# Kernel tuning notes

Hardware: AMD Instinct MI355X
Metric: run time of the kernel (lower is better)

## Reference

```python
import jax, jax.numpy as jnp
import numpy as np

SENSOR_H, SENSOR_W = 256, 256
SPP = 16
BATCH, C, H_IMG, W_IMG = 4, 3, 1024, 1024


def setup_inputs() -> dict:
    key = jax.random.key(0)
    k1, k2 = jax.random.split(key)
    img = jax.random.uniform(k1, (BATCH, C, H_IMG, W_IMG), dtype=jnp.float32)
    jitter = jax.random.uniform(k2, (SPP, SENSOR_H, SENSOR_W, 2), dtype=jnp.float32)
    t = jnp.ones((1,), jnp.float32)
    return {"img": img, "t": t, "jitter": jitter}


def deform(pos, t):
    # Analytic per-axis foveation diffeomorphism [-1,1]^2 -> [-1,1]^2:
    #   f(u) = tanh(t*u)/tanh(t), f'(u) = t*(1 - tanh(t*u)^2)/tanh(t)
    # Jacobian is diagonal, so det = f'(x) * f'(y).
    tt = t[0]
    s = jnp.tanh(tt)
    th = jnp.tanh(tt * pos)
    warped = th / s                      # (..., 2)
    dd = tt * (1.0 - th * th) / s        # diagonal Jacobian entries (..., 2)
    det = dd[..., 0] * dd[..., 1]        # (...)
    return warped, det


def grid_sample_border(img, grid):
    # img: (b,c,H,W); grid: (spp,h,w,2) in [-1,1]
    # bilinear, padding_mode='border', align_corners=False (matches F.grid_sample)
    b, c, H, W = img.shape
    gx = (grid[..., 0] + 1.0) * (W / 2.0) - 0.5
    gy = (grid[..., 1] + 1.0) * (H / 2.0) - 0.5
    gx = jnp.clip(gx, 0.0, W - 1.0)
    gy = jnp.clip(gy, 0.0, H - 1.0)
    x0 = jnp.floor(gx)
    y0 = jnp.floor(gy)
    wx = (gx - x0)[None, None]           # (1,1,spp,h,w)
    wy = (gy - y0)[None, None]
    x0i = jnp.clip(x0.astype(jnp.int32), 0, W - 1)
    y0i = jnp.clip(y0.astype(jnp.int32), 0, H - 1)
    x1i = jnp.clip(x0i + 1, 0, W - 1)
    y1i = jnp.clip(y0i + 1, 0, H - 1)
    # fancy-index gather: result (b,c,spp,h,w); avoids tiling img over (b*spp)
    v00 = img[:, :, y0i, x0i]
    v01 = img[:, :, y0i, x1i]
    v10 = img[:, :, y1i, x0i]
    v11 = img[:, :, y1i, x1i]
    return (v00 * (1 - wx) * (1 - wy) + v01 * wx * (1 - wy)
            + v10 * (1 - wx) * wy + v11 * wx * wy)


def reference(img, t, jitter):
    step_x = 2.0 / SENSOR_W
    step_y = 2.0 / SENSOR_H
    px = jnp.arange(-1.0, 1.0, step_x, dtype=jnp.float32)
    py = jnp.arange(-1.0, 1.0, step_y, dtype=jnp.float32)
    gx, gy = jnp.meshgrid(px, py, indexing='xy')          # (h, w)
    pixel_pos = jnp.stack((gx, gy), axis=-1)[None]        # (1, h, w, 2)
    jit = jitter * jnp.array([step_x, step_y], jnp.float32)
    pos = pixel_pos + jit                                 # (spp, h, w, 2)
    warped, det = deform(pos, t)                          # (spp,h,w,2), (spp,h,w)
    samples = grid_sample_border(img, warped)             # (b, c, spp, h, w)
    weighted = jnp.mean(samples * det[None, None], axis=2)  # (b, c, h, w)
    area = jnp.mean(det, axis=0)[None, None]              # (1, 1, h, w)
    return weighted / area
```

## Files before the change

### kernel.cpp

```cpp
#include <hip/hip_runtime.h>
#include <hip/hip_fp16.h>

#define SPP   16
#define SH    256
#define SW    256
#define HI    1024
#define WI    1024
#define CH    3
#define BATCH 4

#define TS    8
#define MAXD  46
#define PLN   2176
#define NITER 34
#define NTHR  64

#define AS1C(p) ((const __attribute__((address_space(1))) void*)(p))
#define AS3(p)  ((__attribute__((address_space(3))) void*)(p))

__device__ __forceinline__ float fast_tanh(float x) {
    const float e = __expf(2.0f * x);
    return (e - 1.0f) * __builtin_amdgcn_rcpf(e + 1.0f);
}

__global__ __launch_bounds__(NTHR, 4) void foveated_wave8(
    const float* __restrict__ img,
    const float* __restrict__ t_ptr,
    const float* __restrict__ jitter,
    float* __restrict__ out)
{
    __shared__ float lds_f[CH][PLN];

    const int bid  = blockIdx.x;
    const int L    = (bid & 7) * 512 + (bid >> 3);
    const int b    = L >> 10;
    const int rem  = L & 1023;
    const int trow = rem >> 5;
    const int tcol = rem & 31;
    const int sx0  = tcol * TS;
    const int sy0  = trow * TS;

    const int lane = threadIdx.x;
    const int sx   = sx0 + (lane & 7);
    const int sy   = sy0 + (lane >> 3);

    const float step  = 2.0f / 256.0f;
    const float tt    = t_ptr[0];
    const float inv_s = __builtin_amdgcn_rcpf(fast_tanh(tt));

    auto gmap = [&](float p) {
        float g = (fast_tanh(tt * p) * inv_s + 1.0f) * 512.0f - 0.5f;
        return fminf(fmaxf(g, 0.0f), 1023.0f);
    };
    const float pxmin = -1.0f + sx0 * step, pxmax = pxmin + TS * step;
    const float pymin = -1.0f + sy0 * step, pymax = pymin + TS * step;
    const int x_lo = max((int)gmap(pxmin) - 1, 0);
    const int x_hi = min((int)gmap(pxmax) + 2, WI - 1);
    const int y_lo = max((int)gmap(pymin) - 1, 0);
    const int y_hi = min((int)gmap(pymax) + 2, HI - 1);
    const int ncols = x_hi - x_lo + 1;
    const int nrows = y_hi - y_lo + 1;
    const bool fits = (ncols > 0) && (nrows > 0) &&
                      (ncols <= MAXD) && (nrows <= MAXD);

    const size_t plane = (size_t)HI * WI;
    const float* __restrict__ p0 = img + (size_t)(b * CH) * plane;
    const float* __restrict__ p1 = p0 + plane;
    const float* __restrict__ p2 = p1 + plane;

    const float px = -1.0f + sx * step;
    const float py = -1.0f + sy * step;

    const float2* __restrict__ jit2 = (const float2*)jitter;
    const int jbase = sy * SW + sx;
    const float2 jv0  = jit2[jbase +  0 * (SH * SW)];
    const float2 jv1  = jit2[jbase +  1 * (SH * SW)];
    const float2 jv2  = jit2[jbase +  2 * (SH * SW)];
    const float2 jv3  = jit2[jbase +  3 * (SH * SW)];
    const float2 jv4  = jit2[jbase +  4 * (SH * SW)];
    const float2 jv5  = jit2[jbase +  5 * (SH * SW)];
    const float2 jv6  = jit2[jbase +  6 * (SH * SW)];
    const float2 jv7  = jit2[jbase +  7 * (SH * SW)];
    const float2 jv8  = jit2[jbase +  8 * (SH * SW)];
    const float2 jv9  = jit2[jbase +  9 * (SH * SW)];
    const float2 jv10 = jit2[jbase + 10 * (SH * SW)];
    const float2 jv11 = jit2[jbase + 11 * (SH * SW)];
    const float2 jv12 = jit2[jbase + 12 * (SH * SW)];
    const float2 jv13 = jit2[jbase + 13 * (SH * SW)];
    const float2 jv14 = jit2[jbase + 14 * (SH * SW)];
    const float2 jv15 = jit2[jbase + 15 * (SH * SW)];

    float acc0 = 0.0f, acc1 = 0.0f, acc2 = 0.0f, dsum = 0.0f;

    float* __restrict__ P0 = &lds_f[0][0];
    float* __restrict__ P1 = &lds_f[1][0];
    float* __restrict__ P2 = &lds_f[2][0];

    auto sample_lds = [&](float jx, float jy) {
        const float posx = px + jx * step;
        const float posy = py + jy * step;

        const float thx = fast_tanh(tt * posx);
        const float thy = fast_tanh(tt * posy);
        const float ddx = tt * (1.0f - thx * thx) * inv_s;
        const float ddy = tt * (1.0f - thy * thy) * inv_s;
        const float det = ddx * ddy;

        float gx = (thx * inv_s + 1.0f) * 512.0f - 0.5f;
        float gy = (thy * inv_s + 1.0f) * 512.0f - 0.5f;
        gx = fminf(fmaxf(gx, 0.0f), (float)(WI - 1));
        gy = fminf(fmaxf(gy, 0.0f), (float)(HI - 1));

        const int xb = min((int)gx, WI - 2);
        const int yb = min((int)gy, HI - 2);
        const float fx = gx - (float)xb;
        const float fy = gy - (float)yb;

        const float w00 = (1.0f - fx) * (1.0f - fy) * det;
        const float w01 = fx * (1.0f - fy) * det;
        const float w10 = (1.0f - fx) * fy * det;
        const float w11 = fx * fy * det;
        dsum += det;

        const int lidx = (yb - y_lo) * ncols + (xb - x_lo);
        const int l10  = lidx + ncols;

        acc0 += w00 * P0[lidx] + w01 * P0[lidx + 1] + w10 * P0[l10] + w11 * P0[l10 + 1];
        acc1 += w00 * P1[lidx] + w01 * P1[lidx + 1] + w10 * P1[l10] + w11 * P1[l10 + 1];
        acc2 += w00 * P2[lidx] + w01 * P2[lidx + 1] + w10 * P2[l10] + w11 * P2[l10 + 1];
    };

    auto sample_glb = [&](float jx, float jy) {
        const float posx = px + jx * step;
        const float posy = py + jy * step;

        const float thx = fast_tanh(tt * posx);
        const float thy = fast_tanh(tt * posy);
        const float ddx = tt * (1.0f - thx * thx) * inv_s;
        const float ddy = tt * (1.0f - thy * thy) * inv_s;
        const float det = ddx * ddy;

        float gx = (thx * inv_s + 1.0f) * 512.0f - 0.5f;
        float gy = (thy * inv_s + 1.0f) * 512.0f - 0.5f;
        gx = fminf(fmaxf(gx, 0.0f), (float)(WI - 1));
        gy = fminf(fmaxf(gy, 0.0f), (float)(HI - 1));

        const int xb = min((int)gx, WI - 2);
        const int yb = min((int)gy, HI - 2);
        const float fx = gx - (float)xb;
        const float fy = gy - (float)yb;

        const float w00 = (1.0f - fx) * (1.0f - fy) * det;
        const float w01 = fx * (1.0f - fy) * det;
        const float w10 = (1.0f - fx) * fy * det;
        const float w11 = fx * fy * det;
        dsum += det;

        const int i0 = yb * WI + xb;
        const int i1 = i0 + WI;
        { const float a0 = p0[i0], a1 = p0[i0 + 1], c0 = p0[i1], c1 = p0[i1 + 1];
          acc0 += a0 * w00 + a1 * w01 + c0 * w10 + c1 * w11; }
        { const float a0 = p1[i0], a1 = p1[i0 + 1], c0 = p1[i1], c1 = p1[i1 + 1];
          acc1 += a0 * w00 + a1 * w01 + c0 * w10 + c1 * w11; }
        { const float a0 = p2[i0], a1 = p2[i0 + 1], c0 = p2[i1], c1 = p2[i1 + 1];
          acc2 += a0 * w00 + a1 * w01 + c0 * w10 + c1 * w11; }
    };

    if (fits) {
        const int npix  = nrows * ncols;
        const int niter = (npix + 63) >> 6;
        const unsigned mdiv = (1u << 22) / (unsigned)ncols + 1u;
        #pragma unroll
        for (int k = 0; k < NITER; ++k) {
            if (k < niter) {
                int i = k * 64 + lane;
                i = min(i, npix - 1);
                const int r = (int)(((unsigned)i * mdiv) >> 22);
                const int c = i - r * ncols;
                const int g = (y_lo + r) * WI + (x_lo + c);
                __builtin_amdgcn_global_load_lds(AS1C(p0 + g), AS3(P0 + k * 64), 4, 0, 0);
                __builtin_amdgcn_global_load_lds(AS1C(p1 + g), AS3(P1 + k * 64), 4, 0, 0);
                __builtin_amdgcn_global_load_lds(AS1C(p2 + g), AS3(P2 + k * 64), 4, 0, 0);
            }
        }
        asm volatile("s_waitcnt vmcnt(0)" ::: "memory");
        __builtin_amdgcn_sched_barrier(0);

        sample_lds(jv0.x,  jv0.y);   sample_lds(jv1.x,  jv1.y);
        sample_lds(jv2.x,  jv2.y);   sample_lds(jv3.x,  jv3.y);
        sample_lds(jv4.x,  jv4.y);   sample_lds(jv5.x,  jv5.y);
        sample_lds(jv6.x,  jv6.y);   sample_lds(jv7.x,  jv7.y);
        sample_lds(jv8.x,  jv8.y);   sample_lds(jv9.x,  jv9.y);
        sample_lds(jv10.x, jv10.y);  sample_lds(jv11.x, jv11.y);
        sample_lds(jv12.x, jv12.y);  sample_lds(jv13.x, jv13.y);
        sample_lds(jv14.x, jv14.y);  sample_lds(jv15.x, jv15.y);
    } else {
        sample_glb(jv0.x,  jv0.y);   sample_glb(jv1.x,  jv1.y);
        sample_glb(jv2.x,  jv2.y);   sample_glb(jv3.x,  jv3.y);
        sample_glb(jv4.x,  jv4.y);   sample_glb(jv5.x,  jv5.y);
        sample_glb(jv6.x,  jv6.y);   sample_glb(jv7.x,  jv7.y);
        sample_glb(jv8.x,  jv8.y);   sample_glb(jv9.x,  jv9.y);
        sample_glb(jv10.x, jv10.y);  sample_glb(jv11.x, jv11.y);
        sample_glb(jv12.x, jv12.y);  sample_glb(jv13.x, jv13.y);
        sample_glb(jv14.x, jv14.y);  sample_glb(jv15.x, jv15.y);
    }

    const float inv_d = 1.0f / dsum;
    const int pix = sy * SW + sx;
    const size_t ob = (size_t)b * CH * (SH * SW) + pix;
    out[ob]                 = acc0 * inv_d;
    out[ob + (SH * SW)]     = acc1 * inv_d;
    out[ob + 2 * (SH * SW)] = acc2 * inv_d;
}

extern "C" void kernel_launch(void* const* d_in, const int* in_sizes, int n_in,
                              void* d_out, int out_size, void* d_ws, size_t ws_size,
                              hipStream_t stream) {
    const float* img    = (const float*)d_in[0];
    const float* t      = (const float*)d_in[1];
    const float* jitter = (const float*)d_in[2];
    float* out          = (float*)d_out;

    hipLaunchKernelGGL(foveated_wave8, dim3(4096), dim3(NTHR), 0, stream,
                       img, t, jitter, out);
}
```

Before: 103.5 us.

## Stage image tile in LDS as fp16 via register double-buffered loads

Swaps the direct global-to-LDS async copies for ordinary global loads into registers. These are converted to fp16 and stored as a packed half2 R/G plane plus a half B plane, which halves the LDS footprint per block. Loads are software-pipelined in two register batches of eight so conversion overlaps outstanding fetches. Launch bounds drop from 4 to 3 waves per EU. The aim is more resident blocks and fewer LDS bytes per sample, at the cost of fp16 rounding of image values, extra VGPR pressure and conversion ALU work.

```diff
diff --git a/kernel.cpp b/kernel.cpp
--- a/kernel.cpp
+++ b/kernel.cpp
@@ -11,25 +11,22 @@
 
 #define TS    8
 #define MAXD  46
-#define PLN   2176
-#define NITER 34
+#define NPAD  2176
 #define NTHR  64
-
-#define AS1C(p) ((const __attribute__((address_space(1))) void*)(p))
-#define AS3(p)  ((__attribute__((address_space(3))) void*)(p))
 
 __device__ __forceinline__ float fast_tanh(float x) {
     const float e = __expf(2.0f * x);
     return (e - 1.0f) * __builtin_amdgcn_rcpf(e + 1.0f);
 }
 
-__global__ __launch_bounds__(NTHR, 4) void foveated_wave8(
+__global__ __launch_bounds__(NTHR, 3) void foveated_hocc8(
     const float* __restrict__ img,
     const float* __restrict__ t_ptr,
     const float* __restrict__ jitter,
     float* __restrict__ out)
 {
-    __shared__ float lds_f[CH][PLN];
+    __shared__ __half2 RG[NPAD];
+    __shared__ __half  B [NPAD];
 
     const int bid  = blockIdx.x;
     const int L    = (bid & 7) * 512 + (bid >> 3);
@@ -92,10 +89,6 @@
 
     float acc0 = 0.0f, acc1 = 0.0f, acc2 = 0.0f, dsum = 0.0f;
 
-    float* __restrict__ P0 = &lds_f[0][0];
-    float* __restrict__ P1 = &lds_f[1][0];
-    float* __restrict__ P2 = &lds_f[2][0];
-
     auto sample_lds = [&](float jx, float jy) {
         const float posx = px + jx * step;
         const float posy = py + jy * step;
@@ -125,9 +118,18 @@
         const int lidx = (yb - y_lo) * ncols + (xb - x_lo);
         const int l10  = lidx + ncols;
 
-        acc0 += w00 * P0[lidx] + w01 * P0[lidx + 1] + w10 * P0[l10] + w11 * P0[l10 + 1];
-        acc1 += w00 * P1[lidx] + w01 * P1[lidx + 1] + w10 * P1[l10] + w11 * P1[l10 + 1];
-        acc2 += w00 * P2[lidx] + w01 * P2[lidx + 1] + w10 * P2[l10] + w11 * P2[l10 + 1];
+        const float2 f00 = __half22float2(RG[lidx]);
+        const float2 f01 = __half22float2(RG[lidx + 1]);
+        const float2 f10 = __half22float2(RG[l10]);
+        const float2 f11 = __half22float2(RG[l10 + 1]);
+        const float v00 = __half2float(B[lidx]);
+        const float v01 = __half2float(B[lidx + 1]);
+        const float v10 = __half2float(B[l10]);
+        const float v11 = __half2float(B[l10 + 1]);
+
+        acc0 += w00 * f00.x + w01 * f01.x + w10 * f10.x + w11 * f11.x;
+        acc1 += w00 * f00.y + w01 * f01.y + w10 * f10.y + w11 * f11.y;
+        acc2 += w00 * v00   + w01 * v01   + w10 * v10   + w11 * v11;
     };
 
     auto sample_glb = [&](float jx, float jy) {
@@ -170,20 +172,50 @@
         const int npix  = nrows * ncols;
         const int niter = (npix + 63) >> 6;
         const unsigned mdiv = (1u << 22) / (unsigned)ncols + 1u;
-        #pragma unroll
-        for (int k = 0; k < NITER; ++k) {
-            if (k < niter) {
-                int i = k * 64 + lane;
-                i = min(i, npix - 1);
-                const int r = (int)(((unsigned)i * mdiv) >> 22);
-                const int c = i - r * ncols;
-                const int g = (y_lo + r) * WI + (x_lo + c);
-                __builtin_amdgcn_global_load_lds(AS1C(p0 + g), AS3(P0 + k * 64), 4, 0, 0);
-                __builtin_amdgcn_global_load_lds(AS1C(p1 + g), AS3(P1 + k * 64), 4, 0, 0);
-                __builtin_amdgcn_global_load_lds(AS1C(p2 + g), AS3(P2 + k * 64), 4, 0, 0);
+
+        float arA[8], agA[8], abA[8];
+        float arB[8], agB[8], abB[8];
+
+        #define ISSUE(K, CNT, VR, VG, VB)                                   \
+            if ((K) * 8 < niter) {                                          \
+                _Pragma("unroll")                                           \
+                for (int u = 0; u < (CNT); ++u) {                           \
+                    const int it = (K) * 8 + u;                             \
+                    const int ic = min(it * 64 + lane, npix - 1);           \
+                    const int rr = (int)(((unsigned)ic * mdiv) >> 22);      \
+                    const int cc = ic - rr * ncols;                         \
+                    const int g  = (y_lo + rr) * WI + (x_lo + cc);          \
+                    VR[u] = p0[g];                                          \
+                    VG[u] = p1[g];                                          \
+                    VB[u] = p2[g];                                          \
+                }                                                           \
             }
-        }
-        asm volatile("s_waitcnt vmcnt(0)" ::: "memory");
+
+        #define COMMIT(K, CNT, VR, VG, VB)                                  \
+            if ((K) * 8 < niter) {                                          \
+                _Pragma("unroll")                                           \
+                for (int u = 0; u < (CNT); ++u) {                           \
+                    const int i = ((K) * 8 + u) * 64 + lane;                \
+                    RG[i] = __floats2half2_rn(VR[u], VG[u]);                \
+                    B [i] = __float2half_rn(VB[u]);                         \
+                }                                                           \
+            }
+
+        ISSUE (0, 8, arA, agA, abA);
+        ISSUE (1, 8, arB, agB, abB);
+        COMMIT(0, 8, arA, agA, abA);
+        ISSUE (2, 8, arA, agA, abA);
+        COMMIT(1, 8, arB, agB, abB);
+        ISSUE (3, 8, arB, agB, abB);
+        COMMIT(2, 8, arA, agA, abA);
+        ISSUE (4, 2, arA, agA, abA);
+        COMMIT(3, 8, arB, agB, abB);
+        COMMIT(4, 2, arA, agA, abA);
+
+        #undef ISSUE
+        #undef COMMIT
+
+        asm volatile("s_waitcnt lgkmcnt(0)" ::: "memory");
         __builtin_amdgcn_sched_barrier(0);
 
         sample_lds(jv0.x,  jv0.y);   sample_lds(jv1.x,  jv1.y);
@@ -221,6 +253,6 @@
     const float* jitter = (const float*)d_in[2];
     float* out          = (float*)d_out;
 
-    hipLaunchKernelGGL(foveated_wave8, dim3(4096), dim3(NTHR), 0, stream,
+    hipLaunchKernelGGL(foveated_hocc8, dim3(4096), dim3(NTHR), 0, stream,
                        img, t, jitter, out);
 }
```

Result: slower. 106.5 us (+2.9%).

## Stage full image rows per sensor row in fp16 LDS with vector loads

Applied to the files above, without the earlier changes.

Each 256-thread block now handles one whole sensor row instead of an 8x8 tile. It loads the needed input image rows (at most 10) with coalesced float4 loads, double-buffered in registers, and stores them in LDS as packed fp16: red/green in half2, blue as half. This replaces the per-element global_load_lds gather and its index division with wide contiguous loads, and halves LDS footprint and traffic. In exchange, texel values lose precision to fp16. Blocks that need more rows than fit fall back to the global-memory sampling path.

```diff
diff --git a/kernel.cpp b/kernel.cpp
--- a/kernel.cpp
+++ b/kernel.cpp
@@ -9,40 +9,31 @@
 #define CH    3
 #define BATCH 4
 
-#define TS    8
-#define MAXD  46
-#define PLN   2176
-#define NITER 34
-#define NTHR  64
-
-#define AS1C(p) ((const __attribute__((address_space(1))) void*)(p))
-#define AS3(p)  ((__attribute__((address_space(3))) void*)(p))
+#define MAXR  10
+#define RSTR  1028
+#define NTHR  256
 
 __device__ __forceinline__ float fast_tanh(float x) {
     const float e = __expf(2.0f * x);
     return (e - 1.0f) * __builtin_amdgcn_rcpf(e + 1.0f);
 }
 
-__global__ __launch_bounds__(NTHR, 4) void foveated_wave8(
+__global__ __launch_bounds__(NTHR, 2) void foveated_row(
     const float* __restrict__ img,
     const float* __restrict__ t_ptr,
     const float* __restrict__ jitter,
     float* __restrict__ out)
 {
-    __shared__ float lds_f[CH][PLN];
-
-    const int bid  = blockIdx.x;
-    const int L    = (bid & 7) * 512 + (bid >> 3);
-    const int b    = L >> 10;
-    const int rem  = L & 1023;
-    const int trow = rem >> 5;
-    const int tcol = rem & 31;
-    const int sx0  = tcol * TS;
-    const int sy0  = trow * TS;
-
-    const int lane = threadIdx.x;
-    const int sx   = sx0 + (lane & 7);
-    const int sy   = sy0 + (lane >> 3);
+    __shared__ __half2 RG[MAXR * RSTR];
+    __shared__ __half  Bp[MAXR * RSTR];
+
+    const int bid = blockIdx.x;
+    const int L   = (bid & 7) * 128 + (bid >> 3);
+    const int b   = L >> 8;
+    const int sy  = L & 255;
+
+    const int th = threadIdx.x;
+    const int sx = th;
 
     const float step  = 2.0f / 256.0f;
     const float tt    = t_ptr[0];
@@ -52,16 +43,11 @@
         float g = (fast_tanh(tt * p) * inv_s + 1.0f) * 512.0f - 0.5f;
         return fminf(fmaxf(g, 0.0f), 1023.0f);
     };
-    const float pxmin = -1.0f + sx0 * step, pxmax = pxmin + TS * step;
-    const float pymin = -1.0f + sy0 * step, pymax = pymin + TS * step;
-    const int x_lo = max((int)gmap(pxmin) - 1, 0);
-    const int x_hi = min((int)gmap(pxmax) + 2, WI - 1);
-    const int y_lo = max((int)gmap(pymin) - 1, 0);
-    const int y_hi = min((int)gmap(pymax) + 2, HI - 1);
-    const int ncols = x_hi - x_lo + 1;
+    const float pyrow = -1.0f + sy * step;
+    const int y_lo  = max((int)gmap(pyrow) - 1, 0);
+    const int y_hi  = min((int)gmap(pyrow + step) + 2, HI - 1);
     const int nrows = y_hi - y_lo + 1;
-    const bool fits = (ncols > 0) && (nrows > 0) &&
-                      (ncols <= MAXD) && (nrows <= MAXD);
+    const bool fits = (nrows > 0) && (nrows <= MAXR);
 
     const size_t plane = (size_t)HI * WI;
     const float* __restrict__ p0 = img + (size_t)(b * CH) * plane;
@@ -69,7 +55,7 @@
     const float* __restrict__ p2 = p1 + plane;
 
     const float px = -1.0f + sx * step;
-    const float py = -1.0f + sy * step;
+    const float py = pyrow;
 
     const float2* __restrict__ jit2 = (const float2*)jitter;
     const int jbase = sy * SW + sx;
@@ -92,10 +78,6 @@
 
     float acc0 = 0.0f, acc1 = 0.0f, acc2 = 0.0f, dsum = 0.0f;
 
-    float* __restrict__ P0 = &lds_f[0][0];
-    float* __restrict__ P1 = &lds_f[1][0];
-    float* __restrict__ P2 = &lds_f[2][0];
-
     auto sample_lds = [&](float jx, float jy) {
         const float posx = px + jx * step;
         const float posy = py + jy * step;
@@ -122,12 +104,20 @@
         const float w11 = fx * fy * det;
         dsum += det;
 
-        const int lidx = (yb - y_lo) * ncols + (xb - x_lo);
-        const int l10  = lidx + ncols;
-
-        acc0 += w00 * P0[lidx] + w01 * P0[lidx + 1] + w10 * P0[l10] + w11 * P0[l10 + 1];
-        acc1 += w00 * P1[lidx] + w01 * P1[lidx + 1] + w10 * P1[l10] + w11 * P1[l10 + 1];
-        acc2 += w00 * P2[lidx] + w01 * P2[lidx + 1] + w10 * P2[l10] + w11 * P2[l10 + 1];
+        const int o   = (yb - y_lo) * RSTR + xb;
+        const int o1  = o + RSTR;
+        const float2 f00 = __half22float2(RG[o]);
+        const float2 f01 = __half22float2(RG[o + 1]);
+        const float2 f10 = __half22float2(RG[o1]);
+        const float2 f11 = __half22float2(RG[o1 + 1]);
+        const float v00 = __half2float(Bp[o]);
+        const float v01 = __half2float(Bp[o + 1]);
+        const float v10 = __half2float(Bp[o1]);
+        const float v11 = __half2float(Bp[o1 + 1]);
+
+        acc0 += w00 * f00.x + w01 * f01.x + w10 * f10.x + w11 * f11.x;
+        acc1 += w00 * f00.y + w01 * f01.y + w10 * f10.y + w11 * f11.y;
+        acc2 += w00 * v00   + w01 * v01   + w10 * v10   + w11 * v11;
     };
 
     auto sample_glb = [&](float jx, float jy) {
@@ -167,24 +157,56 @@
     };
 
     if (fits) {
-        const int npix  = nrows * ncols;
-        const int niter = (npix + 63) >> 6;
-        const unsigned mdiv = (1u << 22) / (unsigned)ncols + 1u;
-        #pragma unroll
-        for (int k = 0; k < NITER; ++k) {
-            if (k < niter) {
-                int i = k * 64 + lane;
-                i = min(i, npix - 1);
-                const int r = (int)(((unsigned)i * mdiv) >> 22);
-                const int c = i - r * ncols;
-                const int g = (y_lo + r) * WI + (x_lo + c);
-                __builtin_amdgcn_global_load_lds(AS1C(p0 + g), AS3(P0 + k * 64), 4, 0, 0);
-                __builtin_amdgcn_global_load_lds(AS1C(p1 + g), AS3(P1 + k * 64), 4, 0, 0);
-                __builtin_amdgcn_global_load_lds(AS1C(p2 + g), AS3(P2 + k * 64), 4, 0, 0);
+        const int c0 = th * 4;
+        float4 rA, gA, bA, rB, gB, bB;
+
+        #define ISSUE(r, RR, GG, BB)                                         \
+            if ((r) < nrows) {                                               \
+                const float* rowp = p0 + (size_t)(y_lo + (r)) * WI + c0;     \
+                RR = *(const float4*)(rowp);                                 \
+                GG = *(const float4*)(rowp + plane);                         \
+                BB = *(const float4*)(rowp + 2 * plane);                     \
             }
-        }
-        asm volatile("s_waitcnt vmcnt(0)" ::: "memory");
-        __builtin_amdgcn_sched_barrier(0);
+        #define COMMIT(r, RR, GG, BB)                                        \
+            if ((r) < nrows) {                                               \
+                const int o = (r) * RSTR + c0;                               \
+                union { __half2 h[4]; uint4 u; } vv;                         \
+                vv.h[0] = __floats2half2_rn(RR.x, GG.x);                     \
+                vv.h[1] = __floats2half2_rn(RR.y, GG.y);                     \
+                vv.h[2] = __floats2half2_rn(RR.z, GG.z);                     \
+                vv.h[3] = __floats2half2_rn(RR.w, GG.w);                     \
+                *(uint4*)&RG[o] = vv.u;                                      \
+                union { __half2 h[2]; uint2 u; } bb;                         \
+                bb.h[0] = __floats2half2_rn(BB.x, BB.y);                     \
+                bb.h[1] = __floats2half2_rn(BB.z, BB.w);                     \
+                *(uint2*)&Bp[o] = bb.u;                                      \
+            }
+
+        ISSUE (0, rA, gA, bA);
+        ISSUE (1, rB, gB, bB);
+        COMMIT(0, rA, gA, bA);
+        ISSUE (2, rA, gA, bA);
+        COMMIT(1, rB, gB, bB);
+        ISSUE (3, rB, gB, bB);
+        COMMIT(2, rA, gA, bA);
+        ISSUE (4, rA, gA, bA);
+        COMMIT(3, rB, gB, bB);
+        ISSUE (5, rB, gB, bB);
+        COMMIT(4, rA, gA, bA);
+        ISSUE (6, rA, gA, bA);
+        COMMIT(5, rB, gB, bB);
+        ISSUE (7, rB, gB, bB);
+        COMMIT(6, rA, gA, bA);
+        ISSUE (8, rA, gA, bA);
+        COMMIT(7, rB, gB, bB);
+        ISSUE (9, rB, gB, bB);
+        COMMIT(8, rA, gA, bA);
+        COMMIT(9, rB, gB, bB);
+
+        #undef ISSUE
+        #undef COMMIT
+
+        __syncthreads();
 
         sample_lds(jv0.x,  jv0.y);   sample_lds(jv1.x,  jv1.y);
         sample_lds(jv2.x,  jv2.y);   sample_lds(jv3.x,  jv3.y);
@@ -221,6 +243,6 @@
     const float* jitter = (const float*)d_in[2];
     float* out          = (float*)d_out;
 
-    hipLaunchKernelGGL(foveated_wave8, dim3(4096), dim3(NTHR), 0, stream,
+    hipLaunchKernelGGL(foveated_row, dim3(1024), dim3(NTHR), 0, stream,
                        img, t, jitter, out);
 }
```

Result: slower. 111.8 us (+8.1%).
